# Kernel tuning notes

Measured on AMD Instinct MI355X. Metric: run time of the kernel, lower is better.

## Reference

```python
import jax, jax.numpy as jnp
import numpy as np

N_NODES = 50000
N_EDGES = 800000
IN_DIM = 128
HID_DIM = 128
OUT_DIM = 64


def setup_inputs() -> dict:
    key = jax.random.key(0)
    ks = jax.random.split(key, 6)
    x = jax.random.normal(ks[0], (N_NODES, IN_DIM), dtype=jnp.float32)
    edge_index = jax.random.randint(ks[1], (2, N_EDGES), 0, N_NODES, dtype=jnp.int64)
    # per-hop linear weights (torch Linear layout: [out, in], no bias)
    s = 1.0 / np.sqrt(IN_DIM)
    W0 = jax.random.uniform(ks[2], (HID_DIM, IN_DIM), jnp.float32, -s, s)
    W1 = jax.random.uniform(ks[3], (HID_DIM, IN_DIM), jnp.float32, -s, s)
    W2 = jax.random.uniform(ks[4], (HID_DIM, IN_DIM), jnp.float32, -s, s)
    s2 = 1.0 / np.sqrt(HID_DIM * 3)
    Wfc = jax.random.uniform(ks[5], (OUT_DIM, HID_DIM * 3), jnp.float32, -s2, s2)
    return {"x": x, "edge_index": edge_index, "W0": W0, "W1": W1, "W2": W2, "Wfc": Wfc}


def reference(x, edge_index, W0, W1, W2, Wfc):
    N = x.shape[0]
    row, col = edge_index[0], edge_index[1]  # source, target (PyG source_to_target flow)
    # symmetric degree normalization based on in-degree (degree(col, N))
    deg = jax.ops.segment_sum(jnp.ones(row.shape[0], dtype=x.dtype), col, num_segments=N)
    deg_inv_sqrt = jnp.where(deg > 0, jax.lax.rsqrt(jnp.where(deg > 0, deg, 1.0)), 0.0)
    norm = deg_inv_sqrt[row] * deg_inv_sqrt[col]  # [E]
    # NOTE: original code propagates the ORIGINAL x each iteration, so hops 1 and 2
    # both see the 1-hop propagation of x. Faithfully reproduced here.
    px = jax.ops.segment_sum(norm[:, None] * x[row], col, num_segments=N)  # [N, IN_DIM]
    # per-hop linear projections, concat over hops p=[0,1,2]
    h = jnp.concatenate([x @ W0.T, px @ W1.T, px @ W2.T], axis=1)  # [N, 3*HID_DIM]
    return h @ Wfc.T  # [N, OUT_DIM]
```

## Files before the change

### kernel.cpp

```cpp
#include <hip/hip_runtime.h>
#include <hip/hip_bf16.h>

#define N_IN  128
#define N_OUT 64
#define CFB    256
#define MAXNBC 200
#define SLACKC 5120
#define CHUNK  2048
#define PADR   136

typedef __attribute__((ext_vector_type(8))) short short8;
typedef __attribute__((ext_vector_type(4))) float floatx4;
typedef __attribute__((ext_vector_type(2))) float floatx2;

__device__ __forceinline__ unsigned pack_bf16(float a, float b) {
    __hip_bfloat16 ba = __float2bfloat16(a);
    __hip_bfloat16 bb = __float2bfloat16(b);
    unsigned short ua = *(unsigned short*)&ba;
    unsigned short ub = *(unsigned short*)&bb;
    return ((unsigned)ub << 16) | ua;
}
__device__ __forceinline__ unsigned char fp8b(float v) {
    return (unsigned char)(__builtin_amdgcn_cvt_pk_fp8_f32(v, v, 0, false) & 0xff);
}

__global__ __launch_bounds__(256) void fill_scatter(const int* __restrict__ ei,
                                                    int* __restrict__ gcur,
                                                    unsigned* __restrict__ gsorted,
                                                    const float* __restrict__ W0,
                                                    const float* __restrict__ W1,
                                                    const float* __restrict__ W2,
                                                    const float* __restrict__ Wfc,
                                                    __hip_bfloat16* __restrict__ CT,
                                                    int E, int NBC) {
    __shared__ int lcnt[MAXNBC];
    __shared__ int gbase_s[MAXNBC];
    int base = blockIdx.x * CHUNK;
    for (int i = threadIdx.x; i < NBC; i += 256) lcnt[i] = 0;
    __syncthreads();
    int myc[CHUNK / 256];
    #pragma unroll
    for (int q = 0; q < CHUNK / 256; ++q) {
        int e = base + q * 256 + threadIdx.x;
        int c = (e < E) ? ei[E + e] : -1;
        myc[q] = c;
        if (c >= 0) atomicAdd(&lcnt[c >> 8], 1);
    }
    __syncthreads();
    for (int f = threadIdx.x; f < NBC; f += 256) {
        int n = lcnt[f];
        gbase_s[f] = (n > 0) ? (f * SLACKC + atomicAdd(&gcur[f], n)) : 0;
    }
    __syncthreads();
    #pragma unroll
    for (int q = 0; q < CHUNK / 256; ++q) {
        int c = myc[q];
        if (c >= 0) {
            int e = base + q * 256 + threadIdx.x;
            unsigned r = (unsigned)ei[e];
            int p = atomicAdd(&gbase_s[c >> 8], 1);
            if (p < ((c >> 8) + 1) * SLACKC)
                gsorted[p] = ((unsigned)c << 16) | r;
        }
    }
    if (blockIdx.x < 64) {
        int t = blockIdx.x * 256 + threadIdx.x;
        int n = t >> 7;
        int i = t & 127;
        float a = 0.f;
        if (n < 64) {
            for (int k = 0; k < 128; ++k)
                a += Wfc[n * 384 + k] * W0[k * N_IN + i];
        } else {
            int o = n - 64;
            for (int k = 0; k < 128; ++k)
                a += Wfc[o * 384 + 128 + k] * W1[k * N_IN + i]
                   + Wfc[o * 384 + 256 + k] * W2[k * N_IN + i];
        }
        CT[t] = __float2bfloat16(a);
    }
}

__global__ __launch_bounds__(256) void sortgemm_kernel(
        const int* __restrict__ gcur,
        const unsigned* __restrict__ gsorted,
        unsigned short* __restrict__ srow,
        int* __restrict__ offs,
        int* __restrict__ cnt,
        float* __restrict__ dis,
        const float* __restrict__ x,
        const __hip_bfloat16* __restrict__ CT,
        float* __restrict__ out,
        unsigned char* __restrict__ z8,
        int N, int NBC) {
    __shared__ __align__(16) char smem[(64 + 128) * PADR * 2];
    int tid = threadIdx.x;

    if (blockIdx.x < NBC) {
        unsigned* ev = (unsigned*)smem;
        int* c256 = (int*)(smem + SLACKC * 4);
        int* cur  = c256 + 256;
        int* ts   = cur + 256;
        int f = blockIdx.x;
        int lo = f * SLACKC;
        int m = min(gcur[f], SLACKC);
        for (int i = tid; i < m; i += 256) ev[i] = gsorted[lo + i];
        c256[tid] = 0;
        __syncthreads();
        for (int i = tid; i < m; i += 256)
            atomicAdd(&c256[(ev[i] >> 16) & (CFB - 1)], 1);
        __syncthreads();
        int v = c256[tid];
        int xx = v;
        ts[tid] = xx;
        __syncthreads();
        for (int off = 1; off < 256; off <<= 1) {
            int t2 = (tid >= off) ? ts[tid - off] : 0;
            __syncthreads();
            xx += t2; ts[tid] = xx;
            __syncthreads();
        }
        int b = xx - v;
        cur[tid] = b;
        int node = f * CFB + tid;
        if (node < N) {
            offs[node] = lo + b;
            cnt[node] = v;
            dis[node] = v > 0 ? rsqrtf((float)v) : 0.f;
        }
        __syncthreads();
        for (int i = tid; i < m; i += 256) {
            unsigned val = ev[i];
            int cl = (val >> 16) & (CFB - 1);
            int p = atomicAdd(&cur[cl], 1);
            srow[lo + p] = (unsigned short)(val & 0xffffu);
        }
        return;
    }

    unsigned short* xs = (unsigned short*)smem;
    unsigned short* Bs = xs + 64 * PADR;
    int base = (blockIdx.x - NBC) * 64;

    {
        int row = tid >> 2;
        int colq = (tid & 3) * 32;
        int node = base + row;
        unsigned tmp[16];
        if (node < N) {
            const float4* src = (const float4*)(x + (size_t)node * N_IN + colq);
            #pragma unroll
            for (int q = 0; q < 8; ++q) {
                float4 v = src[q];
                tmp[q * 2]     = pack_bf16(v.x, v.y);
                tmp[q * 2 + 1] = pack_bf16(v.z, v.w);
            }
        } else {
            #pragma unroll
            for (int q = 0; q < 16; ++q) tmp[q] = 0u;
        }
        unsigned* dst = (unsigned*)(xs + row * PADR + colq);
        #pragma unroll
        for (int q = 0; q < 16; ++q) dst[q] = tmp[q];
    }
    {
        const unsigned* src = (const unsigned*)CT;
        for (int c = tid; c < 8192; c += 256) {
            int row = c >> 6;
            int col = (c & 63) * 2;
            *(unsigned*)(Bs + row * PADR + col) = src[c];
        }
    }
    __syncthreads();

    int wave = tid >> 6, lane = tid & 63;
    int wm = wave & 1, wn = wave >> 1;
    int quad = lane >> 4, l16 = lane & 15;

    floatx4 acc[2][4];
    #pragma unroll
    for (int mt = 0; mt < 2; ++mt)
        #pragma unroll
        for (int nt = 0; nt < 4; ++nt)
            acc[mt][nt] = (floatx4){0.f, 0.f, 0.f, 0.f};

    #pragma unroll
    for (int kc = 0; kc < 4; ++kc) {
        int kof = kc * 32 + quad * 8;
        short8 afr[2], bfr[4];
        #pragma unroll
        for (int mt = 0; mt < 2; ++mt)
            afr[mt] = *(const short8*)(xs + (wm * 32 + mt * 16 + l16) * PADR + kof);
        #pragma unroll
        for (int nt = 0; nt < 4; ++nt)
            bfr[nt] = *(const short8*)(Bs + (wn * 64 + nt * 16 + l16) * PADR + kof);
        #pragma unroll
        for (int mt = 0; mt < 2; ++mt)
            #pragma unroll
            for (int nt = 0; nt < 4; ++nt)
                acc[mt][nt] = __builtin_amdgcn_mfma_f32_16x16x32_bf16(
                    afr[mt], bfr[nt], acc[mt][nt], 0, 0, 0);
    }

    #pragma unroll
    for (int mt = 0; mt < 2; ++mt) {
        #pragma unroll
        for (int reg = 0; reg < 4; ++reg) {
            int node = base + wm * 32 + mt * 16 + quad * 4 + reg;
            if (node >= N) continue;
            if (wn == 0) {
                #pragma unroll
                for (int nt = 0; nt < 4; ++nt)
                    out[(size_t)node * N_OUT + nt * 16 + l16] = acc[mt][nt][reg];
            } else {
                #pragma unroll
                for (int nt = 0; nt < 4; ++nt)
                    z8[((size_t)node << 6) + nt * 16 + l16] = fp8b(acc[mt][nt][reg]);
            }
        }
    }
}

__global__ __launch_bounds__(256) void gather_kernel(
        const int* __restrict__ offs, const int* __restrict__ cnt,
        const unsigned short* __restrict__ srow, const unsigned char* __restrict__ z8,
        const float* __restrict__ dis, float* __restrict__ out, int N) {
    int node = blockIdx.x * 4 + (threadIdx.x >> 6);
    if (node >= N) return;
    int lane = threadIdx.x & 63;
    int sub  = lane >> 3;
    int jj   = lane & 7;
    int start = offs[node];
    int deg   = cnt[node];
    float a[8] = {0.f, 0.f, 0.f, 0.f, 0.f, 0.f, 0.f, 0.f};
    for (int k0 = 0; k0 < deg; k0 += 64) {
        int m = min(64, deg - k0);
        int idx = 0; float dv = 0.f;
        if (lane < m) {
            idx = (int)srow[start + k0 + lane];
            dv = dis[idx];
        }
        for (int kk = 0; kk < m; kk += 16) {
            int s0 = kk + sub, s1 = kk + 8 + sub;
            int r0 = __shfl(idx, s0); float d0 = __shfl(dv, s0);
            int r1 = __shfl(idx, s1); float d1 = __shfl(dv, s1);
            uint2 u0 = make_uint2(0u, 0u), u1 = make_uint2(0u, 0u);
            if (s0 < m) u0 = *(const uint2*)(z8 + ((size_t)r0 << 6) + jj * 8);
            if (s1 < m) u1 = *(const uint2*)(z8 + ((size_t)r1 << 6) + jj * 8);
            floatx2 p00 = __builtin_amdgcn_cvt_pk_f32_fp8(u0.x, false);
            floatx2 p01 = __builtin_amdgcn_cvt_pk_f32_fp8(u0.x, true);
            floatx2 p02 = __builtin_amdgcn_cvt_pk_f32_fp8(u0.y, false);
            floatx2 p03 = __builtin_amdgcn_cvt_pk_f32_fp8(u0.y, true);
            floatx2 p10 = __builtin_amdgcn_cvt_pk_f32_fp8(u1.x, false);
            floatx2 p11 = __builtin_amdgcn_cvt_pk_f32_fp8(u1.x, true);
            floatx2 p12 = __builtin_amdgcn_cvt_pk_f32_fp8(u1.y, false);
            floatx2 p13 = __builtin_amdgcn_cvt_pk_f32_fp8(u1.y, true);
            a[0] += d0 * p00.x + d1 * p10.x;
            a[1] += d0 * p00.y + d1 * p10.y;
            a[2] += d0 * p01.x + d1 * p11.x;
            a[3] += d0 * p01.y + d1 * p11.y;
            a[4] += d0 * p02.x + d1 * p12.x;
            a[5] += d0 * p02.y + d1 * p12.y;
            a[6] += d0 * p03.x + d1 * p13.x;
            a[7] += d0 * p03.y + d1 * p13.y;
        }
    }
    #pragma unroll
    for (int q = 0; q < 8; ++q) {
        a[q] += __shfl_xor(a[q], 8);
        a[q] += __shfl_xor(a[q], 16);
        a[q] += __shfl_xor(a[q], 32);
    }
    if (lane < 8 && deg > 0) {
        float dn = dis[node];
        float4* op = (float4*)(out + ((size_t)node << 6) + jj * 8);
        float4 o0 = op[0], o1 = op[1];
        o0.x += dn * a[0]; o0.y += dn * a[1]; o0.z += dn * a[2]; o0.w += dn * a[3];
        o1.x += dn * a[4]; o1.y += dn * a[5]; o1.z += dn * a[6]; o1.w += dn * a[7];
        op[0] = o0; op[1] = o1;
    }
}

extern "C" void kernel_launch(void* const* d_in, const int* in_sizes, int n_in,
                              void* d_out, int out_size, void* d_ws, size_t ws_size,
                              hipStream_t stream) {
    const float* x   = (const float*)d_in[0];
    const int*   ei  = (const int*)d_in[1];
    const float* W0  = (const float*)d_in[2];
    const float* W1  = (const float*)d_in[3];
    const float* W2  = (const float*)d_in[4];
    const float* Wfc = (const float*)d_in[5];
    float* out = (float*)d_out;
    int N = in_sizes[0] / N_IN;
    int E = in_sizes[1] / 2;
    int NBC = (N + CFB - 1) / CFB;
    int GB  = (N + 63) / 64;

    __hip_bfloat16* CT = (__hip_bfloat16*)d_ws;
    int*   cnt     = (int*)((char*)d_ws + 32768);
    float* dis     = (float*)(cnt + N);
    int*   gcur    = (int*)(dis + N);
    int*   offs    = gcur + NBC;
    unsigned* gsorted = (unsigned*)(offs + N);
    unsigned short* srow = (unsigned short*)(gsorted + (size_t)NBC * SLACKC);
    size_t zoff = ((size_t)(srow + (size_t)NBC * SLACKC) - (size_t)d_ws + 63) & ~(size_t)63;
    unsigned char* z8 = (unsigned char*)d_ws + zoff;

    hipMemsetAsync(gcur, 0, (size_t)NBC * sizeof(int), stream);
    fill_scatter<<<(E + CHUNK - 1) / CHUNK, 256, 0, stream>>>(ei, gcur, gsorted,
                                                              W0, W1, W2, Wfc, CT, E, NBC);
    sortgemm_kernel<<<NBC + GB, 256, 0, stream>>>(gcur, gsorted, srow, offs, cnt, dis,
                                                  x, CT, out, z8, N, NBC);
    gather_kernel<<<(N + 3) / 4, 256, 0, stream>>>(offs, cnt, srow, z8, dis, out, N);
}
```

Baseline: 144.5 us.

## Fuse three kernels into one persistent kernel with software grid barriers

Merges the scatter, sort/GEMM and gather kernels into a single persistent kernel sized by occupancy, using a hierarchical atomic grid barrier between phases. Work is distributed by grid-stride loops over chunks, buckets/tiles and node groups. The goal is to remove launch gaps and tail effects between the three kernels. In exchange it adds barrier spin overhead and forces a uniform launch-bounds/occupancy setting across phases. It also assumes 256 CUs and that all blocks are co-resident, since the barrier deadlocks otherwise.

```diff
diff --git a/kernel.cpp b/kernel.cpp
--- a/kernel.cpp
+++ b/kernel.cpp
@@ -24,47 +24,84 @@
     return (unsigned char)(__builtin_amdgcn_cvt_pk_fp8_f32(v, v, 0, false) & 0xff);
 }
 
-__global__ __launch_bounds__(256) void fill_scatter(const int* __restrict__ ei,
-                                                    int* __restrict__ gcur,
-                                                    unsigned* __restrict__ gsorted,
-                                                    const float* __restrict__ W0,
-                                                    const float* __restrict__ W1,
-                                                    const float* __restrict__ W2,
-                                                    const float* __restrict__ Wfc,
-                                                    __hip_bfloat16* __restrict__ CT,
-                                                    int E, int NBC) {
-    __shared__ int lcnt[MAXNBC];
-    __shared__ int gbase_s[MAXNBC];
-    int base = blockIdx.x * CHUNK;
-    for (int i = threadIdx.x; i < NBC; i += 256) lcnt[i] = 0;
+__device__ __forceinline__ void grid_barrier(int* bar, int G) {
     __syncthreads();
-    int myc[CHUNK / 256];
-    #pragma unroll
-    for (int q = 0; q < CHUNK / 256; ++q) {
-        int e = base + q * 256 + threadIdx.x;
-        int c = (e < E) ? ei[E + e] : -1;
-        myc[q] = c;
-        if (c >= 0) atomicAdd(&lcnt[c >> 8], 1);
+    if (threadIdx.x == 0) {
+        __threadfence();
+        int gen = __hip_atomic_load(&bar[9], __ATOMIC_RELAXED, __HIP_MEMORY_SCOPE_AGENT);
+        int sub = blockIdx.x & 7;
+        int subn = (G >> 3) + ((sub < (G & 7)) ? 1 : 0);
+        bool release = false;
+        if (atomicAdd(&bar[sub], 1) == subn - 1) {
+            atomicExch(&bar[sub], 0);
+            if (atomicAdd(&bar[8], 1) == 7) {
+                atomicExch(&bar[8], 0);
+                __threadfence();
+                atomicAdd(&bar[9], 1);
+                release = true;
+            }
+        }
+        if (!release) {
+            while (__hip_atomic_load(&bar[9], __ATOMIC_ACQUIRE,
+                                     __HIP_MEMORY_SCOPE_AGENT) == gen)
+                __builtin_amdgcn_s_sleep(8);
+        }
+        __threadfence();
     }
     __syncthreads();
-    for (int f = threadIdx.x; f < NBC; f += 256) {
-        int n = lcnt[f];
-        gbase_s[f] = (n > 0) ? (f * SLACKC + atomicAdd(&gcur[f], n)) : 0;
-    }
-    __syncthreads();
-    #pragma unroll
-    for (int q = 0; q < CHUNK / 256; ++q) {
-        int c = myc[q];
-        if (c >= 0) {
-            int e = base + q * 256 + threadIdx.x;
-            unsigned r = (unsigned)ei[e];
-            int p = atomicAdd(&gbase_s[c >> 8], 1);
-            if (p < ((c >> 8) + 1) * SLACKC)
-                gsorted[p] = ((unsigned)c << 16) | r;
-        }
-    }
-    if (blockIdx.x < 64) {
-        int t = blockIdx.x * 256 + threadIdx.x;
+}
+
+__global__ __launch_bounds__(256, 3) void fused_kernel(
+        const int* __restrict__ ei,
+        int* __restrict__ gcur,
+        int* __restrict__ bar,
+        unsigned* __restrict__ gsorted,
+        const float* __restrict__ W0, const float* __restrict__ W1,
+        const float* __restrict__ W2, const float* __restrict__ Wfc,
+        __hip_bfloat16* __restrict__ CT,
+        unsigned short* __restrict__ srow,
+        int* __restrict__ offs, int* __restrict__ cnt, float* __restrict__ dis,
+        const float* __restrict__ x,
+        float* __restrict__ out, unsigned char* __restrict__ z8,
+        int E, int N, int NBC, int NCH, int GB, int G) {
+    __shared__ __align__(16) char smem[(64 + 128) * PADR * 2];
+    int tid = threadIdx.x;
+
+    for (int ch = blockIdx.x; ch < NCH; ch += G) {
+        int* lcnt = (int*)smem;
+        int* gbase_s = lcnt + MAXNBC;
+        int base = ch * CHUNK;
+        for (int i = tid; i < NBC; i += 256) lcnt[i] = 0;
+        __syncthreads();
+        int myc[CHUNK / 256];
+        #pragma unroll
+        for (int q = 0; q < CHUNK / 256; ++q) {
+            int e = base + q * 256 + tid;
+            int c = (e < E) ? ei[E + e] : -1;
+            myc[q] = c;
+            if (c >= 0) atomicAdd(&lcnt[c >> 8], 1);
+        }
+        __syncthreads();
+        for (int f = tid; f < NBC; f += 256) {
+            int n = lcnt[f];
+            gbase_s[f] = (n > 0) ? (f * SLACKC + atomicAdd(&gcur[f], n)) : 0;
+        }
+        __syncthreads();
+        #pragma unroll
+        for (int q = 0; q < CHUNK / 256; ++q) {
+            int c = myc[q];
+            if (c >= 0) {
+                int e = base + q * 256 + tid;
+                unsigned r = (unsigned)ei[e];
+                int p = atomicAdd(&gbase_s[c >> 8], 1);
+                if (p < ((c >> 8) + 1) * SLACKC)
+                    gsorted[p] = ((unsigned)c << 16) | r;
+            }
+        }
+        __syncthreads();
+    }
+    if ((int)blockIdx.x >= G - 64) {
+        int t = ((int)blockIdx.x - (G - 64)) * 256 + tid;
         int n = t >> 7;
         int i = t & 127;
         float a = 0.f;
@@ -79,205 +116,190 @@
         }
         CT[t] = __float2bfloat16(a);
     }
-}
-
-__global__ __launch_bounds__(256) void sortgemm_kernel(
-        const int* __restrict__ gcur,
-        const unsigned* __restrict__ gsorted,
-        unsigned short* __restrict__ srow,
-        int* __restrict__ offs,
-        int* __restrict__ cnt,
-        float* __restrict__ dis,
-        const float* __restrict__ x,
-        const __hip_bfloat16* __restrict__ CT,
-        float* __restrict__ out,
-        unsigned char* __restrict__ z8,
-        int N, int NBC) {
-    __shared__ __align__(16) char smem[(64 + 128) * PADR * 2];
-    int tid = threadIdx.x;
-
-    if (blockIdx.x < NBC) {
-        unsigned* ev = (unsigned*)smem;
-        int* c256 = (int*)(smem + SLACKC * 4);
-        int* cur  = c256 + 256;
-        int* ts   = cur + 256;
-        int f = blockIdx.x;
-        int lo = f * SLACKC;
-        int m = min(gcur[f], SLACKC);
-        for (int i = tid; i < m; i += 256) ev[i] = gsorted[lo + i];
-        c256[tid] = 0;
-        __syncthreads();
-        for (int i = tid; i < m; i += 256)
-            atomicAdd(&c256[(ev[i] >> 16) & (CFB - 1)], 1);
-        __syncthreads();
-        int v = c256[tid];
-        int xx = v;
-        ts[tid] = xx;
-        __syncthreads();
-        for (int off = 1; off < 256; off <<= 1) {
-            int t2 = (tid >= off) ? ts[tid - off] : 0;
-            __syncthreads();
-            xx += t2; ts[tid] = xx;
-            __syncthreads();
-        }
-        int b = xx - v;
-        cur[tid] = b;
-        int node = f * CFB + tid;
-        if (node < N) {
-            offs[node] = lo + b;
-            cnt[node] = v;
-            dis[node] = v > 0 ? rsqrtf((float)v) : 0.f;
-        }
-        __syncthreads();
-        for (int i = tid; i < m; i += 256) {
-            unsigned val = ev[i];
-            int cl = (val >> 16) & (CFB - 1);
-            int p = atomicAdd(&cur[cl], 1);
-            srow[lo + p] = (unsigned short)(val & 0xffffu);
-        }
-        return;
-    }
-
-    unsigned short* xs = (unsigned short*)smem;
-    unsigned short* Bs = xs + 64 * PADR;
-    int base = (blockIdx.x - NBC) * 64;
-
-    {
-        int row = tid >> 2;
-        int colq = (tid & 3) * 32;
-        int node = base + row;
-        unsigned tmp[16];
-        if (node < N) {
-            const float4* src = (const float4*)(x + (size_t)node * N_IN + colq);
+    grid_barrier(bar, G);
+
+    for (int u = blockIdx.x; u < NBC + GB; u += G) {
+        if (u < NBC) {
+            unsigned* ev = (unsigned*)smem;
+            int* c256 = (int*)(smem + SLACKC * 4);
+            int* cur  = c256 + 256;
+            int* ts   = cur + 256;
+            int f = u;
+            int lo = f * SLACKC;
+            int m = min(gcur[f], SLACKC);
+            for (int i = tid; i < m; i += 256) ev[i] = gsorted[lo + i];
+            c256[tid] = 0;
+            __syncthreads();
+            for (int i = tid; i < m; i += 256)
+                atomicAdd(&c256[(ev[i] >> 16) & (CFB - 1)], 1);
+            __syncthreads();
+            int v = c256[tid];
+            int xx = v;
+            ts[tid] = xx;
+            __syncthreads();
+            for (int off = 1; off < 256; off <<= 1) {
+                int t2 = (tid >= off) ? ts[tid - off] : 0;
+                __syncthreads();
+                xx += t2; ts[tid] = xx;
+                __syncthreads();
+            }
+            int b = xx - v;
+            cur[tid] = b;
+            int node = f * CFB + tid;
+            if (node < N) {
+                offs[node] = lo + b;
+                cnt[node] = v;
+                dis[node] = v > 0 ? rsqrtf((float)v) : 0.f;
+            }
+            __syncthreads();
+            for (int i = tid; i < m; i += 256) {
+                unsigned val = ev[i];
+                int cl = (val >> 16) & (CFB - 1);
+                int p = atomicAdd(&cur[cl], 1);
+                srow[lo + p] = (unsigned short)(val & 0xffffu);
+            }
+        } else {
+            unsigned short* xs = (unsigned short*)smem;
+            unsigned short* Bs = xs + 64 * PADR;
+            int base = (u - NBC) * 64;
+            {
+                int row = tid >> 2;
+                int colq = (tid & 3) * 32;
+                int node = base + row;
+                unsigned tmp[16];
+                if (node < N) {
+                    const float4* src = (const float4*)(x + (size_t)node * N_IN + colq);
+                    #pragma unroll
+                    for (int q = 0; q < 8; ++q) {
+                        float4 vv = src[q];
+                        tmp[q * 2]     = pack_bf16(vv.x, vv.y);
+                        tmp[q * 2 + 1] = pack_bf16(vv.z, vv.w);
+                    }
+                } else {
+                    #pragma unroll
+                    for (int q = 0; q < 16; ++q) tmp[q] = 0u;
+                }
+                unsigned* dst = (unsigned*)(xs + row * PADR + colq);
+                #pragma unroll
+                for (int q = 0; q < 16; ++q) dst[q] = tmp[q];
+            }
+            {
+                const unsigned* src = (const unsigned*)CT;
+                for (int c = tid; c < 8192; c += 256) {
+                    int row = c >> 6;
+                    int col = (c & 63) * 2;
+                    *(unsigned*)(Bs + row * PADR + col) = src[c];
+                }
+            }
+            __syncthreads();
+
+            int wave = tid >> 6, lane = tid & 63;
+            int wm = wave & 1, wn = wave >> 1;
+            int quad = lane >> 4, l16 = lane & 15;
+
+            floatx4 acc[2][4];
             #pragma unroll
-            for (int q = 0; q < 8; ++q) {
-                float4 v = src[q];
-                tmp[q * 2]     = pack_bf16(v.x, v.y);
-                tmp[q * 2 + 1] = pack_bf16(v.z, v.w);
-            }
-        } else {
+            for (int mt = 0; mt < 2; ++mt)
+                #pragma unroll
+                for (int nt = 0; nt < 4; ++nt)
+                    acc[mt][nt] = (floatx4){0.f, 0.f, 0.f, 0.f};
+
             #pragma unroll
-            for (int q = 0; q < 16; ++q) tmp[q] = 0u;
-        }
-        unsigned* dst = (unsigned*)(xs + row * PADR + colq);
-        #pragma unroll
-        for (int q = 0; q < 16; ++q) dst[q] = tmp[q];
-    }
-    {
-        const unsigned* src = (const unsigned*)CT;
-        for (int c = tid; c < 8192; c += 256) {
-            int row = c >> 6;
-            int col = (c & 63) * 2;
-            *(unsigned*)(Bs + row * PADR + col) = src[c];
-        }
-    }
-    __syncthreads();
-
-    int wave = tid >> 6, lane = tid & 63;
-    int wm = wave & 1, wn = wave >> 1;
-    int quad = lane >> 4, l16 = lane & 15;
-
-    floatx4 acc[2][4];
-    #pragma unroll
-    for (int mt = 0; mt < 2; ++mt)
-        #pragma unroll
-        for (int nt = 0; nt < 4; ++nt)
-            acc[mt][nt] = (floatx4){0.f, 0.f, 0.f, 0.f};
-
-    #pragma unroll
-    for (int kc = 0; kc < 4; ++kc) {
-        int kof = kc * 32 + quad * 8;
-        short8 afr[2], bfr[4];
-        #pragma unroll
-        for (int mt = 0; mt < 2; ++mt)
-            afr[mt] = *(const short8*)(xs + (wm * 32 + mt * 16 + l16) * PADR + kof);
-        #pragma unroll
-        for (int nt = 0; nt < 4; ++nt)
-            bfr[nt] = *(const short8*)(Bs + (wn * 64 + nt * 16 + l16) * PADR + kof);
-        #pragma unroll
-        for (int mt = 0; mt < 2; ++mt)
+            for (int kc = 0; kc < 4; ++kc) {
+                int kof = kc * 32 + quad * 8;
+                short8 afr[2], bfr[4];
+                #pragma unroll
+                for (int mt = 0; mt < 2; ++mt)
+                    afr[mt] = *(const short8*)(xs + (wm * 32 + mt * 16 + l16) * PADR + kof);
+                #pragma unroll
+                for (int nt = 0; nt < 4; ++nt)
+                    bfr[nt] = *(const short8*)(Bs + (wn * 64 + nt * 16 + l16) * PADR + kof);
+                #pragma unroll
+                for (int mt = 0; mt < 2; ++mt)
+                    #pragma unroll
+                    for (int nt = 0; nt < 4; ++nt)
+                        acc[mt][nt] = __builtin_amdgcn_mfma_f32_16x16x32_bf16(
+                            afr[mt], bfr[nt], acc[mt][nt], 0, 0, 0);
+            }
+
             #pragma unroll
-            for (int nt = 0; nt < 4; ++nt)
-                acc[mt][nt] = __builtin_amdgcn_mfma_f32_16x16x32_bf16(
-                    afr[mt], bfr[nt], acc[mt][nt], 0, 0, 0);
-    }
-
-    #pragma unroll
-    for (int mt = 0; mt < 2; ++mt) {
-        #pragma unroll
-        for (int reg = 0; reg < 4; ++reg) {
-            int node = base + wm * 32 + mt * 16 + quad * 4 + reg;
-            if (node >= N) continue;
-            if (wn == 0) {
-                #pragma unroll
-                for (int nt = 0; nt < 4; ++nt)
-                    out[(size_t)node * N_OUT + nt * 16 + l16] = acc[mt][nt][reg];
-            } else {
-                #pragma unroll
-                for (int nt = 0; nt < 4; ++nt)
-                    z8[((size_t)node << 6) + nt * 16 + l16] = fp8b(acc[mt][nt][reg]);
-            }
-        }
-    }
-}
-
-__global__ __launch_bounds__(256) void gather_kernel(
-        const int* __restrict__ offs, const int* __restrict__ cnt,
-        const unsigned short* __restrict__ srow, const unsigned char* __restrict__ z8,
-        const float* __restrict__ dis, float* __restrict__ out, int N) {
-    int node = blockIdx.x * 4 + (threadIdx.x >> 6);
-    if (node >= N) return;
-    int lane = threadIdx.x & 63;
+            for (int mt = 0; mt < 2; ++mt) {
+                #pragma unroll
+                for (int reg = 0; reg < 4; ++reg) {
+                    int node = base + wm * 32 + mt * 16 + quad * 4 + reg;
+                    if (node >= N) continue;
+                    if (wn == 0) {
+                        #pragma unroll
+                        for (int nt = 0; nt < 4; ++nt)
+                            out[(size_t)node * N_OUT + nt * 16 + l16] = acc[mt][nt][reg];
+                    } else {
+                        #pragma unroll
+                        for (int nt = 0; nt < 4; ++nt)
+                            z8[((size_t)node << 6) + nt * 16 + l16] = fp8b(acc[mt][nt][reg]);
+                    }
+                }
+            }
+        }
+        __syncthreads();
+    }
+    grid_barrier(bar, G);
+
+    int ngrp = (N + 3) >> 2;
+    int lane = tid & 63;
     int sub  = lane >> 3;
     int jj   = lane & 7;
-    int start = offs[node];
-    int deg   = cnt[node];
-    float a[8] = {0.f, 0.f, 0.f, 0.f, 0.f, 0.f, 0.f, 0.f};
-    for (int k0 = 0; k0 < deg; k0 += 64) {
-        int m = min(64, deg - k0);
-        int idx = 0; float dv = 0.f;
-        if (lane < m) {
-            idx = (int)srow[start + k0 + lane];
-            dv = dis[idx];
-        }
-        for (int kk = 0; kk < m; kk += 16) {
-            int s0 = kk + sub, s1 = kk + 8 + sub;
-            int r0 = __shfl(idx, s0); float d0 = __shfl(dv, s0);
-            int r1 = __shfl(idx, s1); float d1 = __shfl(dv, s1);
-            uint2 u0 = make_uint2(0u, 0u), u1 = make_uint2(0u, 0u);
-            if (s0 < m) u0 = *(const uint2*)(z8 + ((size_t)r0 << 6) + jj * 8);
-            if (s1 < m) u1 = *(const uint2*)(z8 + ((size_t)r1 << 6) + jj * 8);
-            floatx2 p00 = __builtin_amdgcn_cvt_pk_f32_fp8(u0.x, false);
-            floatx2 p01 = __builtin_amdgcn_cvt_pk_f32_fp8(u0.x, true);
-            floatx2 p02 = __builtin_amdgcn_cvt_pk_f32_fp8(u0.y, false);
-            floatx2 p03 = __builtin_amdgcn_cvt_pk_f32_fp8(u0.y, true);
-            floatx2 p10 = __builtin_amdgcn_cvt_pk_f32_fp8(u1.x, false);
-            floatx2 p11 = __builtin_amdgcn_cvt_pk_f32_fp8(u1.x, true);
-            floatx2 p12 = __builtin_amdgcn_cvt_pk_f32_fp8(u1.y, false);
-            floatx2 p13 = __builtin_amdgcn_cvt_pk_f32_fp8(u1.y, true);
-            a[0] += d0 * p00.x + d1 * p10.x;
-            a[1] += d0 * p00.y + d1 * p10.y;
-            a[2] += d0 * p01.x + d1 * p11.x;
-            a[3] += d0 * p01.y + d1 * p11.y;
-            a[4] += d0 * p02.x + d1 * p12.x;
-            a[5] += d0 * p02.y + d1 * p12.y;
-            a[6] += d0 * p03.x + d1 * p13.x;
-            a[7] += d0 * p03.y + d1 * p13.y;
-        }
-    }
-    #pragma unroll
-    for (int q = 0; q < 8; ++q) {
-        a[q] += __shfl_xor(a[q], 8);
-        a[q] += __shfl_xor(a[q], 16);
-        a[q] += __shfl_xor(a[q], 32);
-    }
-    if (lane < 8 && deg > 0) {
-        float dn = dis[node];
-        float4* op = (float4*)(out + ((size_t)node << 6) + jj * 8);
-        float4 o0 = op[0], o1 = op[1];
-        o0.x += dn * a[0]; o0.y += dn * a[1]; o0.z += dn * a[2]; o0.w += dn * a[3];
-        o1.x += dn * a[4]; o1.y += dn * a[5]; o1.z += dn * a[6]; o1.w += dn * a[7];
-        op[0] = o0; op[1] = o1;
+    for (int g = blockIdx.x; g < ngrp; g += G) {
+        int node = g * 4 + (tid >> 6);
+        if (node >= N) continue;
+        int start = offs[node];
+        int deg   = cnt[node];
+        float a[8] = {0.f, 0.f, 0.f, 0.f, 0.f, 0.f, 0.f, 0.f};
+        for (int k0 = 0; k0 < deg; k0 += 64) {
+            int m = min(64, deg - k0);
+            int idx = 0; float dv = 0.f;
+            if (lane < m) {
+                idx = (int)srow[start + k0 + lane];
+                dv = dis[idx];
+            }
+            for (int kk = 0; kk < m; kk += 16) {
+                int s0 = kk + sub, s1 = kk + 8 + sub;
+                int r0 = __shfl(idx, s0); float d0 = __shfl(dv, s0);
+                int r1 = __shfl(idx, s1); float d1 = __shfl(dv, s1);
+                uint2 u0 = make_uint2(0u, 0u), u1 = make_uint2(0u, 0u);
+                if (s0 < m) u0 = *(const uint2*)(z8 + ((size_t)r0 << 6) + jj * 8);
+                if (s1 < m) u1 = *(const uint2*)(z8 + ((size_t)r1 << 6) + jj * 8);
+                floatx2 p00 = __builtin_amdgcn_cvt_pk_f32_fp8(u0.x, false);
+                floatx2 p01 = __builtin_amdgcn_cvt_pk_f32_fp8(u0.x, true);
+                floatx2 p02 = __builtin_amdgcn_cvt_pk_f32_fp8(u0.y, false);
+                floatx2 p03 = __builtin_amdgcn_cvt_pk_f32_fp8(u0.y, true);
+                floatx2 p10 = __builtin_amdgcn_cvt_pk_f32_fp8(u1.x, false);
+                floatx2 p11 = __builtin_amdgcn_cvt_pk_f32_fp8(u1.x, true);
+                floatx2 p12 = __builtin_amdgcn_cvt_pk_f32_fp8(u1.y, false);
+                floatx2 p13 = __builtin_amdgcn_cvt_pk_f32_fp8(u1.y, true);
+                a[0] += d0 * p00.x + d1 * p10.x;
+                a[1] += d0 * p00.y + d1 * p10.y;
+                a[2] += d0 * p01.x + d1 * p11.x;
+                a[3] += d0 * p01.y + d1 * p11.y;
+                a[4] += d0 * p02.x + d1 * p12.x;
+                a[5] += d0 * p02.y + d1 * p12.y;
+                a[6] += d0 * p03.x + d1 * p13.x;
+                a[7] += d0 * p03.y + d1 * p13.y;
+            }
+        }
+        #pragma unroll
+        for (int q = 0; q < 8; ++q) {
+            a[q] += __shfl_xor(a[q], 8);
+            a[q] += __shfl_xor(a[q], 16);
+            a[q] += __shfl_xor(a[q], 32);
+        }
+        if (lane < 8 && deg > 0) {
+            float dn = dis[node];
+            float4* op = (float4*)(out + ((size_t)node << 6) + jj * 8);
+            float4 o0 = op[0], o1 = op[1];
+            o0.x += dn * a[0]; o0.y += dn * a[1]; o0.z += dn * a[2]; o0.w += dn * a[3];
+            o1.x += dn * a[4]; o1.y += dn * a[5]; o1.z += dn * a[6]; o1.w += dn * a[7];
+            op[0] = o0; op[1] = o1;
+        }
     }
 }
 
@@ -294,22 +316,30 @@
     int N = in_sizes[0] / N_IN;
     int E = in_sizes[1] / 2;
     int NBC = (N + CFB - 1) / CFB;
+    int NCH = (E + CHUNK - 1) / CHUNK;
     int GB  = (N + 63) / 64;
 
     __hip_bfloat16* CT = (__hip_bfloat16*)d_ws;
-    int*   cnt     = (int*)((char*)d_ws + 32768);
-    float* dis     = (float*)(cnt + N);
-    int*   gcur    = (int*)(dis + N);
-    int*   offs    = gcur + NBC;
+    int*   cnt  = (int*)((char*)d_ws + 32768);
+    float* dis  = (float*)(cnt + N);
+    int*   gcur = (int*)(dis + N);
+    int*   bar  = gcur + NBC;
+    int*   offs = bar + 16;
     unsigned* gsorted = (unsigned*)(offs + N);
     unsigned short* srow = (unsigned short*)(gsorted + (size_t)NBC * SLACKC);
     size_t zoff = ((size_t)(srow + (size_t)NBC * SLACKC) - (size_t)d_ws + 63) & ~(size_t)63;
     unsigned char* z8 = (unsigned char*)d_ws + zoff;
 
-    hipMemsetAsync(gcur, 0, (size_t)NBC * sizeof(int), stream);
-    fill_scatter<<<(E + CHUNK - 1) / CHUNK, 256, 0, stream>>>(ei, gcur, gsorted,
-                                                              W0, W1, W2, Wfc, CT, E, NBC);
-    sortgemm_kernel<<<NBC + GB, 256, 0, stream>>>(gcur, gsorted, srow, offs, cnt, dis,
-                                                  x, CT, out, z8, N, NBC);
-    gather_kernel<<<(N + 3) / 4, 256, 0, stream>>>(offs, cnt, srow, z8, dis, out, N);
-}
+    int occ = 0;
+    if (hipOccupancyMaxActiveBlocksPerMultiprocessor(
+            &occ, (const void*)fused_kernel, 256, 0) != hipSuccess || occ < 1)
+        occ = 2;
+    int G = occ * 256;
+
+    hipMemsetAsync(gcur, 0, (size_t)(NBC + 16) * sizeof(int), stream);
+    fused_kernel<<<G, 256, 0, stream>>>(ei, gcur, bar, gsorted,
+                                        W0, W1, W2, Wfc, CT,
+                                        srow, offs, cnt, dis,
+                                        x, out, z8,
+                                        E, N, NBC, NCH, GB, G);
+}
```

New measurement: 357.3 us. 2.47x slower.
